# Performance work log

Hardware: AMD Instinct MI355X
Metric: run time of the kernel (lower is better)

## Reference

```python
import jax, jax.numpy as jnp
import numpy as np

B, F_IN, GRID, D, C = 32768, 64, 8, 16, 10
N = GRID * GRID          # 64 nodes
HID = N * D              # 1024
ATOMS = 2
LN_EPS = 1e-5
EPS = 1e-8


def _layernorm(h):
    mu = h.mean(-1, keepdims=True)
    var = h.var(-1, keepdims=True)
    return (h - mu) / jnp.sqrt(var + LN_EPS)


def _regulator(sig, w1, b1, g, be, w2, b2):
    # Linear -> LayerNorm -> Tanh -> Linear -> Sigmoid
    h = jnp.tanh(_layernorm(sig @ w1.T + b1) * g + be)
    return jax.nn.sigmoid(h @ w2.T + b2)


def _reg_params(key, in_dim):
    k = jax.random.split(key, 4)
    return (jax.random.normal(k[0], (16, in_dim)) * 0.3,
            jax.random.normal(k[1], (16,)) * 0.1,
            jnp.ones((16,)), jnp.zeros((16,)),
            jax.random.normal(k[2], (3, 16)) * 0.3,
            jax.random.normal(k[3], (3,)) * 0.1)


def setup_inputs() -> dict:
    key = jax.random.key(0)
    ks = jax.random.split(key, 16)
    # 2D grid 4-neighbour adjacency mask (constant)
    mask = np.zeros((N, N), np.float32)
    for i in range(N):
        r, c = divmod(i, GRID)
        if r > 0: mask[i, i - GRID] = 1
        if r < GRID - 1: mask[i, i + GRID] = 1
        if c > 0: mask[i, i - 1] = 1
        if c < GRID - 1: mask[i, i + 1] = 1
    pr = _reg_params(ks[10], 3)
    cr = _reg_params(ks[11], 3)
    sr = _reg_params(ks[12], 3)
    scr = _reg_params(ks[13], 2)
    inp = {
        "x": jax.random.normal(ks[0], (B, F_IN)),
        "W_embed": jax.random.normal(ks[1], (HID, F_IN)) * 0.1,
        "b_embed": jnp.zeros((HID,)),
        "adj_weights": jax.random.normal(ks[2], (N, N)) * 0.1,
        "adj_mask": jnp.asarray(mask),
        "V_slow": jax.random.normal(ks[3], (D, D)) * 0.1,
        "W_slow": jax.random.normal(ks[4], (D, D)) * 0.1,
        "gate_w": jax.random.normal(ks[5], (1, D)) * 0.3,
        "gate_b": jnp.zeros((1,)),
        "W_fast": jax.random.normal(ks[6], (D, D)) * 0.05,  # buffer, eval mode (no Hebbian update)
        "basis": jax.random.normal(ks[7], (ATOMS, D)) * 0.5,
        "Wq": jax.random.normal(ks[8], (D, D)) * 0.2,
        "sc_w1": jax.random.normal(ks[9], (8, HID)) * 0.05,
        "sc_w2": jax.random.normal(ks[14], (4, 8)) * 0.3,
        "W_read": jax.random.normal(ks[15], (C, HID)) * 0.05,
        "b_read": jnp.zeros((C,)),
    }
    for pre, p in (("pr", pr), ("cr", cr), ("sr", sr), ("scr", scr)):
        for nm, v in zip(("w1", "b1", "g", "be", "w2", "b2"), p):
            inp[pre + "_" + nm] = v
    return inp


def reference(x, W_embed, b_embed, adj_weights, adj_mask,
              pr_w1, pr_b1, pr_g, pr_be, pr_w2, pr_b2,
              V_slow, W_slow, gate_w, gate_b, W_fast,
              cr_w1, cr_b1, cr_g, cr_be, cr_w2, cr_b2,
              basis, Wq,
              sr_w1, sr_b1, sr_g, sr_be, sr_w2, sr_b2,
              sc_w1, sc_w2,
              scr_w1, scr_b1, scr_g, scr_be, scr_w2, scr_b2,
              W_read, b_read):
    Bx = x.shape[0]
    x_embed = (x @ W_embed.T + b_embed).reshape(Bx, N, D)

    # --- AutoregulatedPlasticity adjacency ---
    sig = jnp.stack([jnp.var(x, ddof=1), jnp.abs(x_embed).mean(),
                     jnp.linalg.norm(adj_weights)])[None]
    pl = _regulator(sig, pr_w1, pr_b1, pr_g, pr_be, pr_w2, pr_b2)[0]
    adj = jax.nn.sigmoid(adj_weights * pl[0]) * adj_mask
    adj = adj / jnp.clip(adj.sum(1, keepdims=True), 1e-6, None)
    x_agg = jnp.einsum('nm,bmd->bnd', adj, x_embed)

    # --- AutoregulatedContinuum (eval: W_fast fixed) ---
    xf = x_agg.reshape(-1, D)           # [B*N, D]
    v = xf @ V_slow.T
    sig = jnp.stack([jnp.var(xf, ddof=1), jnp.abs(v).mean(),
                     jnp.linalg.norm(W_slow)])[None]
    ctrl = _regulator(sig, cr_w1, cr_b1, cr_g, cr_be, cr_w2, cr_b2)[0]
    gate = jax.nn.sigmoid(v @ gate_w.T + gate_b) * ctrl[0]   # [B*N, 1]
    fast_out = xf @ W_fast.T
    x_proc = (gate * (v + fast_out * ctrl[2])).reshape(Bx, N, D)

    # --- AutoregulatedSymbiotic, applied per node (vmapped over node axis) ---
    ortho = jnp.linalg.norm(basis @ basis.T - jnp.eye(ATOMS))
    scale = D ** 0.5 + EPS

    def sym_one(xn):  # xn: [B, D]
        w = jax.nn.softmax((xn @ Wq.T) @ basis.T / scale, axis=-1)  # [B, ATOMS]
        ent = -(w * jnp.log(w + EPS)).sum(-1).mean()
        sig_n = jnp.stack([jnp.var(xn, ddof=1), ent, ortho])[None]
        infl = _regulator(sig_n, sr_w1, sr_b1, sr_g, sr_be, sr_w2, sr_b2)[0, 0]
        return (1.0 - infl) * xn + infl * (w @ basis), ent

    refined, ents = jax.vmap(sym_one)(x_proc.transpose(1, 0, 2))  # [N,B,D]
    x_proc = refined.transpose(1, 0, 2)
    entropy = ents[-1]  # torch loop keeps the last node's entropy

    x_flat = x_proc.reshape(Bx, HID)
    logits = x_flat @ W_read.T + b_read

    # --- AutoregulatedSupConHead (entropy.item() -> detached scalar) ---
    sigc = jnp.stack([jnp.var(x_flat, ddof=1),
                      jax.lax.stop_gradient(entropy)])[None]
    gain = _regulator(sigc, scr_w1, scr_b1, scr_g, scr_be, scr_w2, scr_b2)[0, 0]
    proj = (jax.nn.relu(x_flat @ sc_w1.T) @ sc_w2.T) * gain
    return logits, proj, entropy, ortho
```

## Files before the change

kernel.cpp:

```cpp
#include <hip/hip_runtime.h>

typedef unsigned short u16;
typedef unsigned long long u64;
typedef __attribute__((ext_vector_type(8))) short short8;
typedef __attribute__((ext_vector_type(4))) float f32x4;

#define MFMA16(a,b,c) __builtin_amdgcn_mfma_f32_16x16x32_bf16(a,b,c,0,0,0)

#define B_SZ   32768
#define NNODE  64
#define NB_PAIR (B_SZ*NNODE)
#define OUT_PROJ   327680
#define OUT_ENT    458752
#define OUT_ORTHO  458753

#define OFF_SCAL   ((size_t)0)
#define OFF_ADJ    ((size_t)512)
#define OFF_BEFF   (OFF_ADJ  + 8192u)
#define OFF_WEFF   (OFF_BEFF + 4096u)
#define OFF_WCAT   (OFF_WEFF + 131072u)
#define OFF_S1     (OFF_WCAT + 65536u)
#define OFF_S2     (OFF_S1   + 12288u)
#define OFF_S3     (OFF_S2   + 12288u)
#define OFF_S4     (OFF_S3   + 2048u*192u*4u)
#define OFF_H      (OFF_S4   + 8192u)
#define OFF_W01    (OFF_H    + (size_t)B_SZ*8u*4u)
#define OFF_CAN    (OFF_W01  + (size_t)NB_PAIR*4u)

#define CAN_X      0u
#define CAN_WEMB   2097152u
#define CAN_WREAD  (CAN_WEMB + 65536u)
#define CAN_SCW1   (CAN_WREAD + 10240u)
#define CAN_SMALL  (CAN_SCW1 + 8192u)
#define CAN_TOTAL  (CAN_SMALL + 11008u)
#define OFF_BEX    (((OFF_CAN + (size_t)CAN_TOTAL*2u) + 63u) & ~(size_t)63u)
#define OFF_WET    (OFF_BEX + 48u*16u*2u)
#define OFF_VW     (OFF_WET + 131072u)
#define OFF_VB     (OFF_VW  + 131072u)
#define OFF_WC     (OFF_VB  + 4096u)
#define OFF_SW     (OFF_WC  + 131072u)
#define OFF_BC2    (OFF_SW  + 24576u)
#define OFF_SB     (OFF_BC2 + 4096u)
#define OFF_DR     (OFF_SB  + 1024u)
#define WS_NEEDED  (OFF_DR  + 192u*8u)

__device__ __forceinline__ float bf2f(u16 u){
    unsigned v = ((unsigned)u) << 16;
    return __builtin_bit_cast(float, v);
}
__device__ __forceinline__ u16 f2bf(float f){
    unsigned u = __builtin_bit_cast(unsigned, f);
    u += 0x7FFFu + ((u >> 16) & 1u);
    return (u16)(u >> 16);
}
__device__ __forceinline__ float sigm(float x){ return 1.f/(1.f + expf(-x)); }
__device__ __forceinline__ u16 conv_one(const void* src, int i, int isfp32){
    return isfp32 ? f2bf(((const float*)src)[i]) : ((const u16*)src)[i];
}
__device__ __forceinline__ void store_out(void* dout, int idx, float v, int isfp32){
    if (isfp32) ((float*)dout)[idx] = v;
    else        ((u16*)dout)[idx]   = f2bf(v);
}
__device__ __forceinline__ double blk_red(double v, double* sred, int tid){
    #pragma unroll
    for (int off = 32; off > 0; off >>= 1) v += __shfl_xor(v, off);
    if ((tid & 63) == 0) sred[tid >> 6] = v;
    __syncthreads();
    double r = sred[0] + sred[1] + sred[2] + sred[3];
    __syncthreads();
    return r;
}

__device__ void run_regulator(const u16* w1, const u16* b1, const u16* g,
                              const u16* be, const u16* w2, const u16* b2,
                              const float* sig, int in_dim, float* out)
{
    float h[16];
    float mu = 0.f;
    for (int i = 0; i < 16; ++i){
        float a = bf2f(b1[i]);
        for (int j = 0; j < in_dim; ++j) a += sig[j]*bf2f(w1[i*in_dim + j]);
        h[i] = a; mu += a;
    }
    mu *= 0.0625f;
    float var = 0.f;
    for (int i = 0; i < 16; ++i){ float d = h[i]-mu; var += d*d; }
    var *= 0.0625f;
    float inv = 1.f / sqrtf(var + 1e-5f);
    for (int i = 0; i < 16; ++i){
        float hn = (h[i]-mu)*inv;
        h[i] = tanhf(hn*bf2f(g[i]) + bf2f(be[i]));
    }
    for (int c = 0; c < 3; ++c){
        float o = bf2f(b2[c]);
        for (int i = 0; i < 16; ++i) o += h[i]*bf2f(w2[c*16 + i]);
        out[c] = sigm(o);
    }
}

__device__ __forceinline__ int probe_isfp32(const u16* xraw, int tid, int* sred)
{
    int c = 0;
    #pragma unroll
    for (int j = 0; j < 4; ++j){
        u16 u = xraw[(tid*4 + j)*2];
        int e = (u >> 7) & 0xFF;
        if (u == 0 || (e >= 90 && e <= 140)) c++;
    }
    #pragma unroll
    for (int off = 32; off > 0; off >>= 1) c += __shfl_xor(c, off);
    if ((tid & 63) == 0) sred[tid >> 6] = c;
    __syncthreads();
    int tot = sred[0]+sred[1]+sred[2]+sred[3];
    __syncthreads();
    return tot < 614;
}

__global__ __launch_bounds__(256) void kc_big(const void* x, const void* wemb,
    const void* wread, const void* scw1, u16* can, float* scal)
{
    __shared__ int sred[4];
    int tid = threadIdx.x;
    int isfp32 = probe_isfp32((const u16*)x, tid, sred);
    if (blockIdx.x == 0 && tid == 0) scal[127] = isfp32 ? 1.0f : 0.0f;
    int gid = blockIdx.x*256 + tid, stride = gridDim.x*256;
    for (int i = gid; i < 2097152; i += stride) can[CAN_X + i]     = conv_one(x, i, isfp32);
    for (int i = gid; i < 65536;   i += stride) can[CAN_WEMB + i]  = conv_one(wemb, i, isfp32);
    for (int i = gid; i < 10240;   i += stride) can[CAN_WREAD + i] = conv_one(wread, i, isfp32);
    for (int i = gid; i < 8192;    i += stride) can[CAN_SCW1 + i]  = conv_one(scw1, i, isfp32);
}

struct SmallTab { const void* src[36]; int cnt[36]; int off[36]; };
__global__ __launch_bounds__(256) void kc_rest(SmallTab t,
    const void* vslow_raw, const void* gatew_raw,
    const u16* wread, const u16* scw1, const u16* wemb,
    u16* can, const float* scal, u16* wcat, u16* wembT, u16* bex)
{
    int b = blockIdx.x, tid = threadIdx.x;
    int isfp32 = scal[127] != 0.f;
    if (b < 16){
        int gid = b*256 + tid, stride = 16*256;
        for (int e = 0; e < 36; ++e){
            const void* s = t.src[e];
            u16* d = can + t.off[e];
            int n = t.cnt[e];
            for (int i = gid; i < n; i += stride) d[i] = conv_one(s, i, isfp32);
        }
    } else if (b < 144){
        int idx = (b-16)*256 + tid;
        int row = idx >> 10, k = idx & 1023;
        u16 v = 0;
        if (row < 10)      v = wread[row*1024 + k];
        else if (row < 18) v = scw1[(row-10)*1024 + k];
        int lo = k & 31;
        int khw = ((lo >> 2) & 3)*8 + ((lo >> 4) << 2) + (lo & 3);
        wcat[row*1024 + (k & ~31) + khw] = v;
    } else if (b < 400){
        int idx = (b-144)*256 + tid;
        int m = idx >> 10, jj = idx & 1023;
        wembT[jj*64 + m] = wemb[m*1024 + jj];
    } else {
        if (tid < 16){
            float a = 0.f;
            for (int i = 0; i < 16; ++i)
                a += bf2f(conv_one(gatew_raw, i, isfp32))*bf2f(conv_one(vslow_raw, i*16+tid, isfp32));
            bex[32*16+tid] = f2bf(a);
        }
    }
}

__global__ __launch_bounds__(256) void k1_embed(const u16* x, const u16* wemb,
                                                const u16* bemb, float* s1)
{
    __shared__ float red[12];
    int tid = threadIdx.x, wave = tid>>6, lane = tid&63;
    int m = lane&15, quad = lane>>4;
    int cg = blockIdx.x & 31, rc = blockIdx.x >> 5;
    int col0 = cg*32 + m, col1 = col0 + 16;
    short8 b00 = *(const short8*)(wemb + col0*64 + quad*8);
    short8 b01 = *(const short8*)(wemb + col0*64 + quad*8 + 32);
    short8 b10 = *(const short8*)(wemb + col1*64 + quad*8);
    short8 b11 = *(const short8*)(wemb + col1*64 + quad*8 + 32);
    float bias0 = bf2f(bemb[col0]), bias1 = bf2f(bemb[col1]);
    float sx = 0.f, sxx = 0.f, sabs = 0.f;
    const u16* xbase = x + (size_t)(rc*1024 + wave*256 + m)*64 + quad*8;
    #pragma unroll 4
    for (int it = 0; it < 16; ++it){
        const u16* xr = xbase + (size_t)it*16*64;
        short8 a0 = *(const short8*)xr;
        short8 a1 = *(const short8*)(xr + 32);
        if (cg == 0){
            #pragma unroll
            for (int j = 0; j < 8; ++j){
                float f0 = bf2f((u16)a0[j]); sx += f0; sxx += f0*f0;
                float f1 = bf2f((u16)a1[j]); sx += f1; sxx += f1*f1;
            }
        }
        f32x4 zc = {0.f,0.f,0.f,0.f};
        f32x4 c0 = MFMA16(a0, b00, zc);
        c0 = MFMA16(a1, b01, c0);
        f32x4 c1 = MFMA16(a0, b10, zc);
        c1 = MFMA16(a1, b11, c1);
        #pragma unroll
        for (int r = 0; r < 4; ++r)
            sabs += fabsf(c0[r]+bias0) + fabsf(c1[r]+bias1);
    }
    #pragma unroll
    for (int off = 32; off > 0; off >>= 1){
        sx   += __shfl_xor(sx, off);
        sxx  += __shfl_xor(sxx, off);
        sabs += __shfl_xor(sabs, off);
    }
    if (lane == 0){ red[wave*3] = sx; red[wave*3+1] = sxx; red[wave*3+2] = sabs; }
    __syncthreads();
    if (tid == 0){
        for (int k = 0; k < 3; ++k)
            s1[blockIdx.x*3 + k] = red[k] + red[3+k] + red[6+k] + red[9+k];
    }
}

__global__ __launch_bounds__(256) void k2_adj(const u16* adjw, const u16* adjm, const u16* bemb,
    const u16* w1, const u16* b1, const u16* g, const u16* be, const u16* w2, const u16* b2,
    const float* s1, float* scal, u16* adjb, float* beff)
{
    __shared__ double sred[4];
    __shared__ float raw[4096];
    __shared__ float rowsum[64];
    __shared__ float bembs[1024];
    __shared__ float pl0s;
    int tid = threadIdx.x;
    for (int i = tid; i < 1024; i += 256) bembs[i] = bf2f(bemb[i]);
    double s=0, ss=0, sa=0;
    for (int i = tid; i < 1024; i += 256){
        s += (double)s1[i*3]; ss += (double)s1[i*3+1]; sa += (double)s1[i*3+2];
    }
    double nq = 0;
    for (int i = tid; i < 4096; i += 256){ float f = bf2f(adjw[i]); nq += (double)(f*f); }
    double S  = blk_red(s,  sred, tid);
    double SS = blk_red(ss, sred, tid);
    double SA = blk_red(sa, sred, tid);
    double NQ = blk_red(nq, sred, tid);
    if (tid == 0){
        double nx = 2097152.0;
        float sg[3];
        sg[0] = (float)((SS - S*S/nx)/(nx - 1.0));
        sg[1] = (float)(SA / 33554432.0);
        sg[2] = sqrtf((float)NQ);
        float o[3];
        run_regulator(w1,b1,g,be,w2,b2, sg, 3, o);
        scal[0] = o[0]; pl0s = o[0];
    }
    __syncthreads();
    float pl0 = pl0s;
    for (int i = tid; i < 4096; i += 256)
        raw[i] = sigm(bf2f(adjw[i])*pl0) * bf2f(adjm[i]);
    __syncthreads();
    if (tid < 64){
        float r = 0.f;
        for (int mc = 0; mc < 64; ++mc) r += raw[tid*64 + mc];
        rowsum[tid] = fmaxf(r, 1e-6f);
    }
    __syncthreads();
    for (int i = tid; i < 4096; i += 256) adjb[i] = f2bf(raw[i] / rowsum[i>>6]);
    for (int o = tid; o < 1024; o += 256){
        int n = o >> 4, d = o & 15;
        float a = 0.f;
        for (int m = 0; m < 64; ++m) a += raw[n*64+m]*bembs[m*16+d];
        beff[o] = a / rowsum[n];
    }
}

__global__ __launch_bounds__(256) void k2b_mfma(const u16* adjb, const u16* wembT, u16* weff)
{
    int tid = threadIdx.x, wave = tid>>6, lane = tid&63;
    int m = lane&15, quad = lane>>4;
    const u16* ar = adjb + (wave*16 + m)*64 + quad*8;
    short8 a0 = *(const short8*)ar;
    short8 a1 = *(const short8*)(ar + 32);
    int col = blockIdx.x*16 + m;
    const u16* br = wembT + col*64 + quad*8;
    short8 b0 = *(const short8*)br;
    short8 b1 = *(const short8*)(br + 32);
    f32x4 acc = {0.f,0.f,0.f,0.f};
    acc = MFMA16(a0, b0, acc);
    acc = MFMA16(a1, b1, acc);
    #pragma unroll
    for (int r = 0; r < 4; ++r)
        weff[(size_t)(wave*16 + quad*4 + r)*1024 + blockIdx.x*16 + m] = f2bf(acc[r]);
}

__global__ __launch_bounds__(256) void kvw(const u16* vslow, const u16* weff, const float* beff,
                                           u16* vw, float* vbias)
{
    __shared__ float Vs[256];
    int tid = threadIdx.x, b = blockIdx.x;
    Vs[tid] = bf2f(vslow[tid]);
    __syncthreads();
    if (b < 256){
        int idx = b*256 + tid;
        int j = idx >> 6, kf = idx & 63;
        int n = j >> 4, i = j & 15;
        float a = 0.f;
        #pragma unroll
        for (int d = 0; d < 16; ++d) a += Vs[i*16+d]*bf2f(weff[(size_t)(n*16+d)*64 + kf]);
        vw[(size_t)j*64 + kf] = f2bf(a);
    } else {
        int o = (b-256)*256 + tid;
        int n = o >> 4, i = o & 15;
        float a = 0.f;
        #pragma unroll
        for (int d = 0; d < 16; ++d) a += Vs[i*16+d]*beff[n*16+d];
        vbias[o] = a;
    }
}

__global__ __launch_bounds__(256) void k3_stats(const u16* x, const u16* weff, const float* beff,
                                                const u16* vw, const float* vbias, float* s2)
{
    __shared__ float red[12];
    int tid = threadIdx.x, wave = tid>>6, lane = tid&63;
    int m = lane&15, quad = lane>>4;
    int cg = blockIdx.x & 31, rc = blockIdx.x >> 5;
    int col0 = cg*32 + m, col1 = col0 + 16;
    short8 b00 = *(const short8*)(weff + (size_t)col0*64 + quad*8);
    short8 b01 = *(const short8*)(weff + (size_t)col0*64 + quad*8 + 32);
    short8 b10 = *(const short8*)(weff + (size_t)col1*64 + quad*8);
    short8 b11 = *(const short8*)(weff + (size_t)col1*64 + quad*8 + 32);
    short8 v00 = *(const short8*)(vw + (size_t)col0*64 + quad*8);
    short8 v01 = *(const short8*)(vw + (size_t)col0*64 + quad*8 + 32);
    short8 v10 = *(const short8*)(vw + (size_t)col1*64 + quad*8);
    short8 v11 = *(const short8*)(vw + (size_t)col1*64 + quad*8 + 32);
    float be0 = beff[col0], be1 = beff[col1];
    float vb0 = vbias[col0], vb1 = vbias[col1];
    float psum=0.f, pssq=0.f, pabsv=0.f;
    const u16* xbase = x + (size_t)(rc*1024 + wave*256 + m)*64 + quad*8;
    #pragma unroll 4
    for (int it = 0; it < 16; ++it){
        const u16* xr = xbase + (size_t)it*16*64;
        short8 a0 = *(const short8*)xr;
        short8 a1 = *(const short8*)(xr + 32);
        f32x4 zc = {0.f,0.f,0.f,0.f};
        f32x4 c0 = MFMA16(a0, b00, zc);
        c0 = MFMA16(a1, b01, c0);
        f32x4 c1 = MFMA16(a0, b10, zc);
        c1 = MFMA16(a1, b11, c1);
        f32x4 w0 = MFMA16(a0, v00, zc);
        w0 = MFMA16(a1, v01, w0);
        f32x4 w1 = MFMA16(a0, v10, zc);
        w1 = MFMA16(a1, v11, w1);
        #pragma unroll
        for (int r = 0; r < 4; ++r){
            float f0 = c0[r] + be0, f1 = c1[r] + be1;
            psum += f0 + f1; pssq += f0*f0 + f1*f1;
            pabsv += fabsf(w0[r] + vb0) + fabsf(w1[r] + vb1);
        }
    }
    #pragma unroll
    for (int off = 32; off > 0; off >>= 1){
        psum  += __shfl_xor(psum, off);
        pssq  += __shfl_xor(pssq, off);
        pabsv += __shfl_xor(pabsv, off);
    }
    if (lane == 0){ red[wave*3] = psum; red[wave*3+1] = pssq; red[wave*3+2] = pabsv; }
    __syncthreads();
    if (tid == 0){
        for (int k = 0; k < 3; ++k)
            s2[blockIdx.x*3 + k] = red[k] + red[3+k] + red[6+k] + red[9+k];
    }
}

__global__ __launch_bounds__(256) void k3b_ctrl(const u16* wslow,
    const u16* vslow, const u16* wfast, const u16* wq, const u16* basis,
    const u16* w1, const u16* b1, const u16* g, const u16* be, const u16* w2, const u16* b2,
    const float* s2, float* scal, u16* bex)
{
    __shared__ double sred[4];
    __shared__ float ctrl2s;
    int tid = threadIdx.x;
    double s=0, ss=0, sv=0;
    for (int i = tid; i < 1024; i += 256){
        s += (double)s2[i*3]; ss += (double)s2[i*3+1]; sv += (double)s2[i*3+2];
    }
    float wf = bf2f(wslow[tid]);
    double nq = (double)(wf*wf);
    double S  = blk_red(s,  sred, tid);
    double SS = blk_red(ss, sred, tid);
    double SV = blk_red(sv, sred, tid);
    double NQ = blk_red(nq, sred, tid);
    if (tid == 0){
        double M = 33554432.0;
        float sg[3];
        sg[0] = (float)((SS - S*S/M)/(M - 1.0));
        sg[1] = (float)(SV / M);
        sg[2] = sqrtf((float)NQ);
        float o[3];
        run_regulator(w1,b1,g,be,w2,b2, sg, 3, o);
        scal[1] = o[0]; scal[2] = o[2];
        ctrl2s = o[2];
    }
    __syncthreads();
    float ctrl2 = ctrl2s;
    if (tid < 64){
        #pragma unroll
        for (int j = 0; j < 4; ++j){
            int idx = tid*4 + j;
            int d = idx >> 4, k = idx & 15;
            bex[(16+d)*16+k] = f2bf(bf2f(vslow[idx]) + ctrl2*bf2f(wfast[idx]));
        }
    } else if (tid < 96){
        int a = (tid-64) >> 4, k = (tid-64) & 15;
        float e = 0.f;
        for (int d = 0; d < 16; ++d){
            float bq = 0.f;
            for (int j = 0; j < 16; ++j) bq += bf2f(basis[a*16+j])*bf2f(wq[j*16+d]);
            e += bq*(bf2f(vslow[d*16+k]) + ctrl2*bf2f(wfast[d*16+k]));
        }
        bex[(33+a)*16+k] = f2bf(0.25f*e);
    }
}

__global__ __launch_bounds__(256) void kbw(const u16* bex, const u16* weff, const float* beff,
                                           const u16* gateb, u16* wc, u16* sw,
                                           float* bc, float* sb)
{
    __shared__ float BcL[256], gvL[16], e0L[16], e1L[16];
    int tid = threadIdx.x;
    if (tid < 256) BcL[tid] = bf2f(bex[(16 + (tid>>4))*16 + (tid&15)]);
    if (tid < 16){
        gvL[tid] = bf2f(bex[32*16+tid]);
        e0L[tid] = bf2f(bex[33*16+tid]);
        e1L[tid] = bf2f(bex[34*16+tid]);
    }
    __syncthreads();
    int id = blockIdx.x*256 + tid;
    if (id < 65536){
        int col = id >> 6, k = id & 63;
        int n = col >> 4, d = col & 15;
        float a = 0.f;
        #pragma unroll
        for (int dd = 0; dd < 16; ++dd)
            a += BcL[d*16+dd]*bf2f(weff[(size_t)(n*16+dd)*64 + k]);
        wc[(size_t)col*64 + k] = f2bf(a);
    } else if (id < 77824){
        int j2 = id - 65536;
        int scol = j2 >> 6, k = j2 & 63;
        int n = scol/3, j = scol - n*3;
        const float* sr = (j==0) ? gvL : (j==1) ? e0L : e1L;
        float a = 0.f;
        #pragma unroll
        for (int dd = 0; dd < 16; ++dd)
            a += sr[dd]*bf2f(weff[(size_t)(n*16+dd)*64 + k]);
        sw[(size_t)scol*64 + k] = f2bf(a);
    } else if (id < 78848){
        int col = id - 77824;
        int n = col >> 4, d = col & 15;
        float a = 0.f;
        #pragma unroll
        for (int dd = 0; dd < 16; ++dd) a += BcL[d*16+dd]*beff[n*16+dd];
        bc[col] = a;
    } else if (id < 79040){
        int s = id - 78848;
        int n = s/3, j = s - n*3;
        const float* sr = (j==0) ? gvL : (j==1) ? e0L : e1L;
        float a = 0.f;
        #pragma unroll
        for (int dd = 0; dd < 16; ++dd) a += sr[dd]*beff[n*16+dd];
        if (j == 0) a += bf2f(gateb[0]);
        sb[s] = a;
    }
}

#define SCP 193
__global__ __launch_bounds__(256) void k4_stats(const u16* x, const u16* wc, const u16* sw,
    const float* bc, const float* sb, const float* scal, unsigned* wpack, float* s3)
{
    __shared__ float sc[16*SCP];
    __shared__ float gt[1024];
    __shared__ float entp[256];
    __shared__ float snode[128];
    int tid = threadIdx.x, wave = tid>>6, lane = tid&63;
    int m = lane&15, quad = lane>>4;
    int row0 = blockIdx.x*16;
    const u16* xr = x + (row0 + m)*64 + quad*8;
    short8 a0 = *(const short8*)xr;
    short8 a1 = *(const short8*)(xr + 32);
    float ctrl0 = scal[1];
    #pragma unroll
    for (int tt = 0; tt < 3; ++tt){
        int ct = wave*3 + tt;
        int scol = ct*16 + m;
        const u16* br = sw + (size_t)scol*64 + quad*8;
        short8 b0 = *(const short8*)br;
        short8 b1 = *(const short8*)(br + 32);
        f32x4 zc = {0.f,0.f,0.f,0.f};
        f32x4 c = MFMA16(a0, b0, zc);
        c = MFMA16(a1, b1, c);
        float sbv = sb[scol];
        #pragma unroll
        for (int r = 0; r < 4; ++r)
            sc[(quad*4+r)*SCP + scol] = c[r] + sbv;
    }
    __syncthreads();
    {
        int n = tid & 63, rgrp = tid >> 6;
        float ent = 0.f;
        #pragma unroll
        for (int rr = 0; rr < 4; ++rr){
            int row = rgrp*4 + rr;
            float gd  = sc[row*SCP + 3*n];
            float e0d = sc[row*SCP + 3*n + 1];
            float e1d = sc[row*SCP + 3*n + 2];
            float gate = ctrl0 / (1.f + __expf(-gd));
            float l0 = gate*e0d, l1 = gate*e1d;
            float w1v = 1.f/(1.f + __expf(l0 - l1));
            float w0v = 1.f - w1v;
            ent += -(w0v*__logf(w0v + 1e-8f) + w1v*__logf(w1v + 1e-8f));
            gt[row*64 + n] = gate;
            wpack[(size_t)(row0 + row)*64 + n] =
                ((unsigned)f2bf(w0v) << 16) | (unsigned)f2bf(gate);
        }
        entp[tid] = ent;
    }
    __syncthreads();
    #pragma unroll
    for (int tt = 0; tt < 16; ++tt){
        int n = wave*16 + tt;
        int col = n*16 + m;
        const u16* br = wc + (size_t)col*64 + quad*8;
        short8 b0 = *(const short8*)br;
        short8 b1 = *(const short8*)(br + 32);
        f32x4 zc = {0.f,0.f,0.f,0.f};
        f32x4 c = MFMA16(a0, b0, zc);
        c = MFMA16(a1, b1, c);
        float bcv = bc[col];
        float ps = 0.f, pq = 0.f;
        #pragma unroll
        for (int r = 0; r < 4; ++r){
            float gate = gt[(quad*4+r)*64 + n];
            float xp = gate*(c[r] + bcv);
            ps += xp; pq += xp*xp;
        }
        #pragma unroll
        for (int off = 32; off > 0; off >>= 1){
            ps += __shfl_xor(ps, off);
            pq += __shfl_xor(pq, off);
        }
        if (lane == 0){ snode[n] = ps; snode[64+n] = pq; }
    }
    __syncthreads();
    if (tid < 192){
        float v;
        if (tid < 128) v = snode[tid];
        else { int n = tid-128; v = entp[n]+entp[64+n]+entp[128+n]+entp[192+n]; }
        s3[(size_t)blockIdx.x*192 + tid] = v;
    }
}

__global__ __launch_bounds__(256) void k5a_red(const float* s3, double* dred)
{
    __shared__ double sred[4];
    int tid = threadIdx.x, col = blockIdx.x;
    double a = 0;
    for (int i = tid; i < 2048; i += 256) a += (double)s3[(size_t)i*192 + col];
    #pragma unroll
    for (int off = 32; off > 0; off >>= 1) a += __shfl_xor(a, off);
    if ((tid & 63) == 0) sred[tid >> 6] = a;
    __syncthreads();
    if (tid == 0) dred[col] = sred[0]+sred[1]+sred[2]+sred[3];
}

__global__ __launch_bounds__(64) void k5b_infl(const u16* basis,
    const u16* w1, const u16* b1, const u16* g, const u16* be, const u16* w2, const u16* b2,
    const double* dred, float* scal, void* dout)
{
    int n = threadIdx.x;
    int isfp32 = scal[127] != 0.f;
    double sum = dred[n], ssq = dred[64+n], ent = dred[128+n];
    double Mn = 524288.0;
    float varn = (float)((ssq - sum*sum/Mn)/(Mn - 1.0));
    float entm = (float)(ent / 32768.0);
    float b0[16], b1v[16];
    for (int d = 0; d < 16; ++d){ b0[d] = bf2f(basis[d]); b1v[d] = bf2f(basis[16+d]); }
    float g00=0.f, g01=0.f, g11=0.f;
    for (int d = 0; d < 16; ++d){ g00 += b0[d]*b0[d]; g01 += b0[d]*b1v[d]; g11 += b1v[d]*b1v[d]; }
    float ortho = sqrtf((g00-1.f)*(g00-1.f) + 2.f*g01*g01 + (g11-1.f)*(g11-1.f));
    float sg[3] = {varn, entm, ortho};
    float o[3];
    run_regulator(w1,b1,g,be,w2,b2, sg, 3, o);
    scal[4+n] = o[0];
    if (n == 63){ scal[68] = entm;  store_out(dout, OUT_ENT,   entm,  isfp32); }
    if (n == 0) { scal[69] = ortho; store_out(dout, OUT_ORTHO, ortho, isfp32); }
}

__global__ __launch_bounds__(128, 4) void k6_read(const u16* x, const unsigned* wpack,
    const u16* wc, const float* bc, const u16* wcatP,
    const u16* basis, const u16* bread, const float* scal,
    void* dout, float* hbuf, float* s4)
{
    __shared__ unsigned gwP[32*65];
    __shared__ float bc_s[1024];
    __shared__ float infl_s[64], b0s[16], b1s[16], brd[16];
    __shared__ float red[4];
    int tid = threadIdx.x;
    int isfp32 = scal[127] != 0.f;
    for (int i = tid; i < 2048; i += 128)
        gwP[(i >> 6)*65 + (i & 63)] = wpack[(size_t)blockIdx.x*2048 + i];
    for (int i = tid; i < 1024; i += 128) bc_s[i] = bc[i];
    if (tid < 64) infl_s[tid] = scal[4+tid];
    if (tid < 16){
        b0s[tid] = bf2f(basis[tid]);
        b1s[tid] = bf2f(basis[16+tid]);
        brd[tid] = (tid < 10) ? bf2f(bread[tid]) : 0.f;
    }
    __syncthreads();
    int wave = tid>>6, lane = tid&63;
    int m = lane&15, quad = lane>>4;
    int row = blockIdx.x*32 + wave*16 + m;
    const u16* xr = x + (size_t)row*64 + quad*8;
    short8 a0 = *(const short8*)xr;
    short8 a1 = *(const short8*)(xr + 32);
    float b0d[4], b1d[4];
    #pragma unroll
    for (int r = 0; r < 4; ++r){ b0d[r] = b0s[quad*4+r]; b1d[r] = b1s[quad*4+r]; }
    const unsigned* gwrow = gwP + (wave*16 + m)*65;
    f32x4 acc0 = {0.f,0.f,0.f,0.f}, acc1 = {0.f,0.f,0.f,0.f};
    float psum = 0.f, pssq = 0.f;
    for (int c8 = 0; c8 < 8; ++c8){
        unsigned pda[8], pdb[8];
        #pragma unroll
        for (int hf = 0; hf < 2; ++hf){
            f32x4 cT[4], bc4[4];
            unsigned gv[4];
            float fiv[4];
            #pragma unroll
            for (int j = 0; j < 4; ++j){
                int n = c8*8 + hf*4 + j;
                int col = n*16 + m;
                const u16* br = wc + (size_t)col*64 + quad*8;
                short8 wf0 = *(const short8*)br;
                short8 wf1 = *(const short8*)(br + 32);
                f32x4 zc = {0.f,0.f,0.f,0.f};
                f32x4 cc = MFMA16(wf0, a0, zc);
                cc = MFMA16(wf1, a1, cc);
                cT[j] = cc;
                bc4[j] = *(const f32x4*)(bc_s + n*16 + quad*4);
                gv[j]  = gwrow[n];
                fiv[j] = infl_s[n];
            }
            #pragma unroll
            for (int j = 0; j < 4; ++j){
                int t = hf*4 + j;
                float gate = bf2f((u16)(gv[j] & 0xFFFFu));
                float w0v  = bf2f((u16)(gv[j] >> 16));
                float fi = fiv[j];
                float A   = (1.f - fi)*gate;
                float fw0 = fi*w0v;
                float fw1 = fi - fw0;
                float xf[4];
                #pragma unroll
                for (int r = 0; r < 4; ++r){
                    float base = fw0*b0d[r] + fw1*b1d[r];
                    float v = A*(cT[j][r] + bc4[j][r]) + base;
                    psum += v; pssq += v*v;
                    xf[r] = v;
                }
                pda[t] = (unsigned)f2bf(xf[0]) | ((unsigned)f2bf(xf[1]) << 16);
                pdb[t] = (unsigned)f2bf(xf[2]) | ((unsigned)f2bf(xf[3]) << 16);
            }
        }
        #pragma unroll
        for (int kk = 0; kk < 4; ++kk){
            int4 aw = make_int4((int)pda[2*kk], (int)pdb[2*kk],
                                (int)pda[2*kk+1], (int)pdb[2*kk+1]);
            short8 af = __builtin_bit_cast(short8, aw);
            const u16* wb = wcatP + m*1024 + c8*128 + kk*32 + quad*8;
            short8 bb0 = *(const short8*)wb;
            short8 bb1 = *(const short8*)(wb + 16*1024);
            acc0 = MFMA16(af, bb0, acc0);
            acc1 = MFMA16(af, bb1, acc1);
        }
    }
    int rowbase = blockIdx.x*32 + wave*16 + quad*4;
    #pragma unroll
    for (int r = 0; r < 4; ++r){
        int rowg = rowbase + r;
        if (m < 10) store_out(dout, rowg*10 + m, acc0[r] + brd[m], isfp32);
        else        hbuf[rowg*8 + (m-10)] = fmaxf(acc0[r], 0.f);
        if (m < 2)  hbuf[rowg*8 + 6 + m]  = fmaxf(acc1[r], 0.f);
    }
    #pragma unroll
    for (int off = 32; off > 0; off >>= 1){
        psum += __shfl_xor(psum, off);
        pssq += __shfl_xor(pssq, off);
    }
    if (lane == 0){ red[wave] = psum; red[2+wave] = pssq; }
    __syncthreads();
    if (tid == 0){
        s4[blockIdx.x*2]   = red[0]+red[1];
        s4[blockIdx.x*2+1] = red[2]+red[3];
    }
}

__global__ __launch_bounds__(256) void k8_proj(const float* hbuf, const u16* scw2,
    const u16* w1, const u16* b1, const u16* g, const u16* be, const u16* w2, const u16* b2,
    const float* s4, const float* scal, void* dout)
{
    __shared__ double sred[4];
    __shared__ float w2s[32];
    __shared__ float gains;
    int tid = threadIdx.x;
    int isfp32 = scal[127] != 0.f;
    if (tid < 32) w2s[tid] = bf2f(scw2[tid]);
    double s=0, ss=0;
    for (int i = tid; i < 1024; i += 256){ s += (double)s4[i*2]; ss += (double)s4[i*2+1]; }
    double S  = blk_red(s,  sred, tid);
    double SS = blk_red(ss, sred, tid);
    if (tid == 0){
        double M = 33554432.0;
        float sg[2];
        sg[0] = (float)((SS - S*S/M)/(M - 1.0));
        sg[1] = scal[68];
        float o[3];
        run_regulator(w1,b1,g,be,w2,b2, sg, 2, o);
        gains = o[0];
    }
    __syncthreads();
    float gain = gains;
    int b = blockIdx.x*256 + tid;
    const float* h = hbuf + (size_t)b*8;
    float hv[8];
    #pragma unroll
    for (int k = 0; k < 8; ++k) hv[k] = h[k];
    #pragma unroll
    for (int i = 0; i < 4; ++i){
        float o = 0.f;
        #pragma unroll
        for (int k = 0; k < 8; ++k) o += hv[k]*w2s[i*8+k];
        store_out(dout, OUT_PROJ + b*4 + i, o*gain, isfp32);
    }
}

extern "C" void kernel_launch(void* const* d_in, const int* in_sizes, int n_in,
                              void* d_out, int out_size, void* d_ws, size_t ws_size,
                              hipStream_t stream)
{
    if (ws_size < WS_NEEDED) return;

    char* ws = (char*)d_ws;
    float* scal  = (float*)(ws + OFF_SCAL);
    u16*   adjb  = (u16*)  (ws + OFF_ADJ);
    float* beff  = (float*)(ws + OFF_BEFF);
    u16*   weff  = (u16*)  (ws + OFF_WEFF);
    u16*   wcat  = (u16*)  (ws + OFF_WCAT);
    float* s1    = (float*)(ws + OFF_S1);
    float* s2    = (float*)(ws + OFF_S2);
    float* s3    = (float*)(ws + OFF_S3);
    float* s4    = (float*)(ws + OFF_S4);
    float* hbuf  = (float*)(ws + OFF_H);
    unsigned* wpack = (unsigned*)(ws + OFF_W01);
    u16*   can   = (u16*)  (ws + OFF_CAN);
    u16*   bex   = (u16*)  (ws + OFF_BEX);
    u16*   wembT = (u16*)  (ws + OFF_WET);
    u16*   vw    = (u16*)  (ws + OFF_VW);
    float* vbias = (float*)(ws + OFF_VB);
    u16*   wc    = (u16*)  (ws + OFF_WC);
    u16*   sw    = (u16*)  (ws + OFF_SW);
    float* bc    = (float*)(ws + OFF_BC2);
    float* sb    = (float*)(ws + OFF_SB);
    double* dred = (double*)(ws + OFF_DR);

    static const int sidx[36] = {2,3,4,5,6,7,8,9,10,11,13,15,
        16,17,18,19,20,21, 22,23,24,25,26,27, 28,29,30,31,32,33, 34,35,36,37,38,39};
    static const int scnt[36] = {1024,4096,4096,256,256,16,1,256,32,256,32,10,
        48,16,16,16,48,3, 48,16,16,16,48,3, 48,16,16,16,48,3, 32,16,16,16,48,3};
    SmallTab t;
    const u16* canp[40];
    {
        int off = (int)CAN_SMALL;
        for (int j = 0; j < 36; ++j){
            t.src[j] = d_in[sidx[j]];
            t.cnt[j] = scnt[j];
            t.off[j] = off;
            canp[sidx[j]] = can + off;
            off += (scnt[j] + 7) & ~7;
        }
    }
    canp[0]  = can + CAN_X;
    canp[1]  = can + CAN_WEMB;
    canp[12] = can + CAN_SCW1;
    canp[14] = can + CAN_WREAD;

    const u16* pr_[6]; const u16* cr_[6]; const u16* sr_[6]; const u16* sc_[6];
    for (int i = 0; i < 6; ++i){
        pr_[i] = canp[16+i]; cr_[i] = canp[22+i];
        sr_[i] = canp[28+i]; sc_[i] = canp[34+i];
    }

    kc_big  <<<1024,256, 0, stream>>>(d_in[0], d_in[1], d_in[14], d_in[12], can, scal);
    kc_rest <<<401, 256, 0, stream>>>(t, d_in[5], d_in[7], canp[14], canp[12], canp[1],
                 can, scal, wcat, wembT, bex);
    k1_embed<<<1024,256, 0, stream>>>(canp[0], canp[1], canp[2], s1);
    k2_adj  <<<1,   256, 0, stream>>>(canp[3], canp[4], canp[2],
                 pr_[0],pr_[1],pr_[2],pr_[3],pr_[4],pr_[5], s1, scal, adjb, beff);
    k2b_mfma<<<64,  256, 0, stream>>>(adjb, wembT, weff);
    kvw     <<<260, 256, 0, stream>>>(canp[5], weff, beff, vw, vbias);
    k3_stats<<<1024,256, 0, stream>>>(canp[0], weff, beff, vw, vbias, s2);
    k3b_ctrl<<<1,   256, 0, stream>>>(canp[6], canp[5], canp[9], canp[11], canp[10],
                 cr_[0],cr_[1],cr_[2],cr_[3],cr_[4],cr_[5], s2, scal, bex);
    kbw     <<<312, 256, 0, stream>>>(bex, weff, beff, canp[8], wc, sw, bc, sb);
    k4_stats<<<2048,256, 0, stream>>>(canp[0], wc, sw, bc, sb, scal, wpack, s3);
    k5a_red <<<192, 256, 0, stream>>>(s3, dred);
    k5b_infl<<<1,   64,  0, stream>>>(canp[10],
                 sr_[0],sr_[1],sr_[2],sr_[3],sr_[4],sr_[5], dred, scal, d_out);
    k6_read <<<1024,128, 0, stream>>>(canp[0], wpack, wc, bc, wcat, canp[10], canp[15],
                 scal, d_out, hbuf, s4);
    k8_proj <<<128, 256, 0, stream>>>(hbuf, canp[13],
                 sc_[0],sc_[1],sc_[2],sc_[3],sc_[4],sc_[5], s4, scal, d_out);
}
```

Before: 342.6 us.

## Fuse influence regulator into readout kernel and batch weight loads per chunk

Removes the single-block k5b_infl launch and recomputes the per-node influence regulator redundantly in every k6_read block from the reduced statistics, with block 0 writing the entropy and ortho outputs. The inner loop of k6_read now issues all eight weight-fragment loads and all sixteen MFMAs per chunk before the elementwise stage, instead of two halves of four, to expose more memory-level and MFMA parallelism. Launch bounds drop from 4 to 2 minimum blocks per SM so the larger register footprint fits. This trades a kernel launch and a dependency bubble for redundant regulator work in each block and possibly lower occupancy. scal[69] (ortho) is no longer written to the scal buffer, which could matter if a later kernel reads it.

```diff
diff --git a/kernel.cpp b/kernel.cpp
--- a/kernel.cpp
+++ b/kernel.cpp
@@ -569,33 +569,12 @@
     if (tid == 0) dred[col] = sred[0]+sred[1]+sred[2]+sred[3];
 }
 
-__global__ __launch_bounds__(64) void k5b_infl(const u16* basis,
-    const u16* w1, const u16* b1, const u16* g, const u16* be, const u16* w2, const u16* b2,
-    const double* dred, float* scal, void* dout)
-{
-    int n = threadIdx.x;
-    int isfp32 = scal[127] != 0.f;
-    double sum = dred[n], ssq = dred[64+n], ent = dred[128+n];
-    double Mn = 524288.0;
-    float varn = (float)((ssq - sum*sum/Mn)/(Mn - 1.0));
-    float entm = (float)(ent / 32768.0);
-    float b0[16], b1v[16];
-    for (int d = 0; d < 16; ++d){ b0[d] = bf2f(basis[d]); b1v[d] = bf2f(basis[16+d]); }
-    float g00=0.f, g01=0.f, g11=0.f;
-    for (int d = 0; d < 16; ++d){ g00 += b0[d]*b0[d]; g01 += b0[d]*b1v[d]; g11 += b1v[d]*b1v[d]; }
-    float ortho = sqrtf((g00-1.f)*(g00-1.f) + 2.f*g01*g01 + (g11-1.f)*(g11-1.f));
-    float sg[3] = {varn, entm, ortho};
-    float o[3];
-    run_regulator(w1,b1,g,be,w2,b2, sg, 3, o);
-    scal[4+n] = o[0];
-    if (n == 63){ scal[68] = entm;  store_out(dout, OUT_ENT,   entm,  isfp32); }
-    if (n == 0) { scal[69] = ortho; store_out(dout, OUT_ORTHO, ortho, isfp32); }
-}
-
-__global__ __launch_bounds__(128, 4) void k6_read(const u16* x, const unsigned* wpack,
+__global__ __launch_bounds__(128, 2) void k6_read(const u16* x, const unsigned* wpack,
     const u16* wc, const float* bc, const u16* wcatP,
-    const u16* basis, const u16* bread, const float* scal,
-    void* dout, float* hbuf, float* s4)
+    const u16* basis, const u16* bread,
+    const u16* rw1, const u16* rb1, const u16* rg, const u16* rbe,
+    const u16* rw2, const u16* rb2, const double* dred,
+    float* scal, void* dout, float* hbuf, float* s4)
 {
     __shared__ unsigned gwP[32*65];
     __shared__ float bc_s[1024];
@@ -606,11 +585,32 @@
     for (int i = tid; i < 2048; i += 128)
         gwP[(i >> 6)*65 + (i & 63)] = wpack[(size_t)blockIdx.x*2048 + i];
     for (int i = tid; i < 1024; i += 128) bc_s[i] = bc[i];
-    if (tid < 64) infl_s[tid] = scal[4+tid];
     if (tid < 16){
         b0s[tid] = bf2f(basis[tid]);
         b1s[tid] = bf2f(basis[16+tid]);
         brd[tid] = (tid < 10) ? bf2f(bread[tid]) : 0.f;
+    }
+    if (tid < 64){
+        int n = tid;
+        double sum = dred[n], ssq = dred[64+n], ent = dred[128+n];
+        double Mn = 524288.0;
+        float varn = (float)((ssq - sum*sum/Mn)/(Mn - 1.0));
+        float entm = (float)(ent / 32768.0);
+        float bb0[16], bb1[16];
+        for (int d = 0; d < 16; ++d){ bb0[d] = bf2f(basis[d]); bb1[d] = bf2f(basis[16+d]); }
+        float g00=0.f, g01=0.f, g11=0.f;
+        for (int d = 0; d < 16; ++d){
+            g00 += bb0[d]*bb0[d]; g01 += bb0[d]*bb1[d]; g11 += bb1[d]*bb1[d];
+        }
+        float ortho = sqrtf((g00-1.f)*(g00-1.f) + 2.f*g01*g01 + (g11-1.f)*(g11-1.f));
+        float sg[3] = {varn, entm, ortho};
+        float o[3];
+        run_regulator(rw1,rb1,rg,rbe,rw2,rb2, sg, 3, o);
+        infl_s[n] = o[0];
+        if (blockIdx.x == 0){
+            if (n == 63){ scal[68] = entm; store_out(dout, OUT_ENT, entm, isfp32); }
+            if (n == 0)  store_out(dout, OUT_ORTHO, ortho, isfp32);
+        }
     }
     __syncthreads();
     int wave = tid>>6, lane = tid&63;
@@ -626,47 +626,52 @@
     f32x4 acc0 = {0.f,0.f,0.f,0.f}, acc1 = {0.f,0.f,0.f,0.f};
     float psum = 0.f, pssq = 0.f;
     for (int c8 = 0; c8 < 8; ++c8){
+        const u16* wbase = wc + (size_t)(c8*8*16 + m)*64 + quad*8;
+        short8 wf0[8], wf1[8];
+        #pragma unroll
+        for (int j = 0; j < 8; ++j){
+            const u16* br = wbase + (size_t)j*16*64;
+            wf0[j] = *(const short8*)br;
+            wf1[j] = *(const short8*)(br + 32);
+        }
+        f32x4 bc4[8];
+        unsigned gv[8];
+        float fiv[8];
+        #pragma unroll
+        for (int j = 0; j < 8; ++j){
+            int n = c8*8 + j;
+            bc4[j] = *(const f32x4*)(bc_s + n*16 + quad*4);
+            gv[j]  = gwrow[n];
+            fiv[j] = infl_s[n];
+        }
+        f32x4 cT[8];
+        #pragma unroll
+        for (int j = 0; j < 8; ++j){
+            f32x4 zc = {0.f,0.f,0.f,0.f};
+            cT[j] = MFMA16(wf0[j], a0, zc);
+        }
+        #pragma unroll
+        for (int j = 0; j < 8; ++j)
+            cT[j] = MFMA16(wf1[j], a1, cT[j]);
         unsigned pda[8], pdb[8];
         #pragma unroll
-        for (int hf = 0; hf < 2; ++hf){
-            f32x4 cT[4], bc4[4];
-            unsigned gv[4];
-            float fiv[4];
+        for (int j = 0; j < 8; ++j){
+            float gate = bf2f((u16)(gv[j] & 0xFFFFu));
+            float w0v  = bf2f((u16)(gv[j] >> 16));
+            float fi = fiv[j];
+            float A   = (1.f - fi)*gate;
+            float fw0 = fi*w0v;
+            float fw1 = fi - fw0;
+            float xf[4];
             #pragma unroll
-            for (int j = 0; j < 4; ++j){
-                int n = c8*8 + hf*4 + j;
-                int col = n*16 + m;
-                const u16* br = wc + (size_t)col*64 + quad*8;
-                short8 wf0 = *(const short8*)br;
-                short8 wf1 = *(const short8*)(br + 32);
-                f32x4 zc = {0.f,0.f,0.f,0.f};
-                f32x4 cc = MFMA16(wf0, a0, zc);
-                cc = MFMA16(wf1, a1, cc);
-                cT[j] = cc;
-                bc4[j] = *(const f32x4*)(bc_s + n*16 + quad*4);
-                gv[j]  = gwrow[n];
-                fiv[j] = infl_s[n];
+            for (int r = 0; r < 4; ++r){
+                float base = fw0*b0d[r] + fw1*b1d[r];
+                float v = A*(cT[j][r] + bc4[j][r]) + base;
+                psum += v; pssq += v*v;
+                xf[r] = v;
             }
-            #pragma unroll
-            for (int j = 0; j < 4; ++j){
-                int t = hf*4 + j;
-                float gate = bf2f((u16)(gv[j] & 0xFFFFu));
-                float w0v  = bf2f((u16)(gv[j] >> 16));
-                float fi = fiv[j];
-                float A   = (1.f - fi)*gate;
-                float fw0 = fi*w0v;
-                float fw1 = fi - fw0;
-                float xf[4];
-                #pragma unroll
-                for (int r = 0; r < 4; ++r){
-                    float base = fw0*b0d[r] + fw1*b1d[r];
-                    float v = A*(cT[j][r] + bc4[j][r]) + base;
-                    psum += v; pssq += v*v;
-                    xf[r] = v;
-                }
-                pda[t] = (unsigned)f2bf(xf[0]) | ((unsigned)f2bf(xf[1]) << 16);
-                pdb[t] = (unsigned)f2bf(xf[2]) | ((unsigned)f2bf(xf[3]) << 16);
-            }
+            pda[j] = (unsigned)f2bf(xf[0]) | ((unsigned)f2bf(xf[1]) << 16);
+            pdb[j] = (unsigned)f2bf(xf[2]) | ((unsigned)f2bf(xf[3]) << 16);
         }
         #pragma unroll
         for (int kk = 0; kk < 4; ++kk){
@@ -810,9 +815,8 @@
     kbw     <<<312, 256, 0, stream>>>(bex, weff, beff, canp[8], wc, sw, bc, sb);
     k4_stats<<<2048,256, 0, stream>>>(canp[0], wc, sw, bc, sb, scal, wpack, s3);
     k5a_red <<<192, 256, 0, stream>>>(s3, dred);
-    k5b_infl<<<1,   64,  0, stream>>>(canp[10],
-                 sr_[0],sr_[1],sr_[2],sr_[3],sr_[4],sr_[5], dred, scal, d_out);
     k6_read <<<1024,128, 0, stream>>>(canp[0], wpack, wc, bc, wcat, canp[10], canp[15],
+                 sr_[0],sr_[1],sr_[2],sr_[3],sr_[4],sr_[5], dred,
                  scal, d_out, hbuf, s4);
     k8_proj <<<128, 256, 0, stream>>>(hbuf, canp[13],
                  sc_[0],sc_[1],sc_[2],sc_[3],sc_[4],sc_[5], s4, scal, d_out);
```

Result: slower. 352.4 us (+2.9%).
